# Kernel tuning notes

Hardware: AMD Instinct MI355X
Metric: run time of the kernel (lower is better)

Reference implementation:

```python
import jax, jax.numpy as jnp
import numpy as np

M, K, N = 4096, 4096, 4096

def setup_inputs() -> dict:
    key = jax.random.key(0)
    k1, k2, k3 = jax.random.split(key, 3)
    a = jax.random.randint(k1, (M, K), 0, 127, dtype=jnp.int32)
    b = jax.random.randint(k2, (K, N), 0, 127, dtype=jnp.int32)
    scale = jax.random.uniform(k3, (N,), dtype=jnp.float32)
    return {"a": a, "b": b, "scale": scale}

def reference(a, b, scale):
    a8 = a.astype(jnp.int8)
    b8 = b.astype(jnp.int8)
    acc = jnp.matmul(a8, b8, preferred_element_type=jnp.int32)  # [M, N] int32
    # fused per-column (per-output-channel) dequantization scale
    return acc.astype(jnp.float32) * scale[None, :]  # [M, N] float32
```

## Files before the change

### kernel.cpp

```cpp
#include <hip/hip_runtime.h>
#include <stdint.h>

#define M_DIM 4096
#define K_DIM 4096
#define N_DIM 4096

typedef int v4i __attribute__((ext_vector_type(4)));
typedef int int32x4 __attribute__((ext_vector_type(4)));

__device__ __forceinline__ void gload_lds16(const void* g, void* l) {
    __builtin_amdgcn_global_load_lds(
        (const __attribute__((address_space(1))) uint32_t*)g,
        (__attribute__((address_space(3))) uint32_t*)l, 16, 0, 0);
}

__global__ void pack_a_kernel(const int* __restrict__ a, char* __restrict__ a8, int total4) {
    int idx = blockIdx.x * blockDim.x + threadIdx.x;
    int stride = gridDim.x * blockDim.x;
    for (int i = idx; i < total4; i += stride) {
        int32x4 v = ((const int32x4*)a)[i];
        uint32_t p = (uint32_t)(v.x & 0xff) | ((uint32_t)(v.y & 0xff) << 8) |
                     ((uint32_t)(v.z & 0xff) << 16) | ((uint32_t)(v.w & 0xff) << 24);
        ((uint32_t*)a8)[i] = p;
    }
}

__global__ void pack_bt_kernel(const int* __restrict__ b, char* __restrict__ b8t) {
    __shared__ char tile[64][68];
    int k0 = blockIdx.y * 64;
    int n0 = blockIdx.x * 64;
    int tx = threadIdx.x & 63;
    int ty = threadIdx.x >> 6;
#pragma unroll
    for (int kk = 0; kk < 64; kk += 4) {
        tile[kk + ty][tx] = (char)b[(size_t)(k0 + kk + ty) * N_DIM + n0 + tx];
    }
    __syncthreads();
    int td = threadIdx.x & 15;
    int tn = threadIdx.x >> 4;
#pragma unroll
    for (int nn0 = 0; nn0 < 64; nn0 += 16) {
        int nn = nn0 + tn;
        uint32_t p = (uint32_t)(uint8_t)tile[td * 4 + 0][nn] |
                     ((uint32_t)(uint8_t)tile[td * 4 + 1][nn] << 8) |
                     ((uint32_t)(uint8_t)tile[td * 4 + 2][nn] << 16) |
                     ((uint32_t)(uint8_t)tile[td * 4 + 3][nn] << 24);
        *(uint32_t*)&b8t[(size_t)(n0 + nn) * K_DIM + k0 + td * 4] = p;
    }
}

#define BM 256
#define BN 256
#define BK 128
#define KTILES (K_DIM / BK)

#define BAR __builtin_amdgcn_s_barrier()
#define WAIT_LGKM asm volatile("s_waitcnt lgkmcnt(0)" ::: "memory")
#define WAIT_VM4 asm volatile("s_waitcnt vmcnt(4)" ::: "memory")
#define WAIT_VM0 asm volatile("s_waitcnt vmcnt(0)" ::: "memory")

#define DS_A(dst, kk, ib)                                                               \
    _Pragma("unroll") for (int i_ = 0; i_ < 4; ++i_) dst[i_] =                          \
        *(const v4i*)(lds + bufOff + (kk) * 16384 + aOff + ((ib) + i_) * 1024);

#define DS_B(dst, kk)                                                                   \
    _Pragma("unroll") for (int j_ = 0; j_ < 4; ++j_) dst[j_] =                          \
        *(const v4i*)(lds + bufOff + (kk) * 16384 + bOff + j_ * 1024);

#define MM(ib, AF, BF)                                                                  \
    __builtin_amdgcn_s_setprio(1);                                                      \
    _Pragma("unroll") for (int i_ = 0; i_ < 4; ++i_)                                    \
    _Pragma("unroll") for (int j_ = 0; j_ < 4; ++j_)                                    \
        acc[(ib) + i_][j_] =                                                            \
            __builtin_amdgcn_mfma_i32_16x16x64_i8(AF[i_], BF[j_], acc[(ib) + i_][j_],   \
                                                  0, 0, 0);                             \
    __builtin_amdgcn_s_setprio(0);

__global__ __launch_bounds__(512, 2) void gemm_i8_8ph(const char* __restrict__ A8,
                                                      const char* __restrict__ B8T,
                                                      const float* __restrict__ scale,
                                                      float* __restrict__ out) {
    __shared__ char lds[131072];

    int tid = threadIdx.x;
    int wave = tid >> 6;
    int lane = tid & 63;
    int wr = wave >> 2;
    int wc = wave & 3;
    int l15 = lane & 15;

    int bid = blockIdx.x;
    int swz = (bid & 7) * 32 + (bid >> 3);
    int bm = swz >> 4;
    int bn = swz & 15;

    int rA = tid >> 2;
    int cc = ((tid & 3) ^ ((tid >> 3) & 3)) << 4;
    const char* aSrc = A8 + (size_t)(bm * BM + rA) * K_DIM + cc;
    const char* bSrc = B8T + (size_t)(bn * BN + rA) * K_DIM + cc;

    int slot = (((lane >> 4) ^ ((lane >> 1) & 3)) << 4);
    int aOff = wr * 8192 + l15 * 64 + slot;
    int bOff = 32768 + wc * 4096 + l15 * 64 + slot;

    v4i acc[8][4];
#pragma unroll
    for (int i = 0; i < 8; ++i)
#pragma unroll
        for (int j = 0; j < 4; ++j) acc[i][j] = (v4i){0, 0, 0, 0};

    auto stage = [&](const char* srcBase, int kt1, int kk, int dstOff) {
        const char* s = srcBase + (size_t)kt1 * BK + kk * 64;
        char* d = (char*)lds + dstOff + wave * 1024;
        gload_lds16(s, d);
        gload_lds16(s + (size_t)128 * K_DIM, d + 8192);
    };

    stage(aSrc, 0, 0, 0);
    stage(bSrc, 0, 0, 32768);
    stage(aSrc, 0, 1, 16384);
    stage(bSrc, 0, 1, 49152);
    WAIT_VM4;
    BAR;

    int bufOff = 0;
    v4i aF[4], aG[4], bF[4];

    for (int kt = 0; kt < KTILES - 1; ++kt) {
        int nbufOff = bufOff ^ 65536;
        DS_A(aF, 0, 0);
        DS_B(bF, 0);
        stage(aSrc, kt + 1, 0, nbufOff + 0);
        BAR;
        WAIT_LGKM;
        MM(0, aF, bF);
        BAR;
        DS_A(aG, 0, 4);
        stage(bSrc, kt + 1, 0, nbufOff + 32768);
        BAR;
        WAIT_LGKM;
        MM(4, aG, bF);
        WAIT_VM4;
        BAR;
        DS_A(aF, 1, 0);
        DS_B(bF, 1);
        stage(aSrc, kt + 1, 1, nbufOff + 16384);
        BAR;
        WAIT_LGKM;
        MM(0, aF, bF);
        BAR;
        DS_A(aG, 1, 4);
        stage(bSrc, kt + 1, 1, nbufOff + 49152);
        BAR;
        WAIT_LGKM;
        MM(4, aG, bF);
        WAIT_VM4;
        BAR;
        bufOff = nbufOff;
    }

    DS_A(aF, 0, 0);
    DS_B(bF, 0);
    BAR;
    WAIT_LGKM;
    MM(0, aF, bF);
    BAR;
    DS_A(aG, 0, 4);
    BAR;
    WAIT_LGKM;
    MM(4, aG, bF);
    WAIT_VM0;
    BAR;
    DS_A(aF, 1, 0);
    DS_B(bF, 1);
    BAR;
    WAIT_LGKM;
    MM(0, aF, bF);
    BAR;
    DS_A(aG, 1, 4);
    WAIT_LGKM;
    MM(4, aG, bF);

    size_t orow0 = (size_t)bm * BM + wr * 128 + (lane >> 4) * 4;
    int ocol0 = bn * BN + wc * 64 + l15;
#pragma unroll
    for (int j = 0; j < 4; ++j) {
        int col = ocol0 + j * 16;
        float s = scale[col];
#pragma unroll
        for (int i = 0; i < 8; ++i) {
            size_t row = orow0 + (size_t)i * 16;
#pragma unroll
            for (int r = 0; r < 4; ++r) {
                out[(row + r) * N_DIM + col] = (float)acc[i][j][r] * s;
            }
        }
    }
}

#define FBM 128
#define FBN 128
#define FBK 64

__global__ __launch_bounds__(256) void gemm_i8_fused_kernel(const int* __restrict__ a,
                                                            const int* __restrict__ b,
                                                            const float* __restrict__ scale,
                                                            float* __restrict__ out) {
    __shared__ char As[FBM * FBK];
    __shared__ char Bs[FBN * FBK];

    int tid = threadIdx.x;
    int wave = tid >> 6;
    int lane = tid & 63;

    int nwg = gridDim.x;
    int cpx = nwg >> 3;
    int bid = blockIdx.x;
    int swz = (bid & 7) * cpx + (bid >> 3);
    int bm = swz >> 5;
    int bn = swz & 31;

    int f0 = tid * 16;
    int m0 = f0 >> 6;
    int k0 = f0 & 63;

    int nn = tid & 127;
    int kh = tid >> 7;

    int wr = wave >> 1;
    int wc = wave & 1;
    int lrow = lane & 15;
    int kgrp = (lane >> 4) * 16;

    v4i acc[4][4];
#pragma unroll
    for (int i = 0; i < 4; ++i)
#pragma unroll
        for (int j = 0; j < 4; ++j) acc[i][j] = (v4i){0, 0, 0, 0};

    const int kTiles = K_DIM / FBK;
    for (int kt = 0; kt < kTiles; ++kt) {
        __syncthreads();
#pragma unroll
        for (int r = 0; r < 2; ++r) {
            const int* src = a + (size_t)(bm * FBM + m0 + r * 64) * K_DIM + kt * FBK + k0;
            uint32_t pk[4];
#pragma unroll
            for (int q = 0; q < 4; ++q) {
                int32x4 v = *(const int32x4*)(src + q * 4);
                pk[q] = (uint32_t)(v.x & 0xff) | ((uint32_t)(v.y & 0xff) << 8) |
                        ((uint32_t)(v.z & 0xff) << 16) | ((uint32_t)(v.w & 0xff) << 24);
            }
            *(v4i*)&As[f0 + r * 4096] = (v4i){(int)pk[0], (int)pk[1], (int)pk[2], (int)pk[3]};
        }
#pragma unroll
        for (int d = 0; d < 8; ++d) {
            uint32_t p = 0;
#pragma unroll
            for (int i = 0; i < 4; ++i) {
                int kk = kt * FBK + kh * 32 + d * 4 + i;
                p |= (uint32_t)(b[(size_t)kk * N_DIM + bn * FBN + nn] & 0xff) << (8 * i);
            }
            *(uint32_t*)&Bs[nn * 64 + kh * 32 + d * 4] = p;
        }
        __syncthreads();

        v4i aF[4], bF[4];
#pragma unroll
        for (int i = 0; i < 4; ++i)
            aF[i] = *(const v4i*)&As[(wr * 64 + i * 16 + lrow) * FBK + kgrp];
#pragma unroll
        for (int j = 0; j < 4; ++j)
            bF[j] = *(const v4i*)&Bs[(wc * 64 + j * 16 + lrow) * FBK + kgrp];
#pragma unroll
        for (int i = 0; i < 4; ++i)
#pragma unroll
            for (int j = 0; j < 4; ++j)
                acc[i][j] = __builtin_amdgcn_mfma_i32_16x16x64_i8(aF[i], bF[j], acc[i][j], 0, 0, 0);
    }

    size_t orow0 = (size_t)bm * FBM + wr * 64;
    int ocol0 = bn * FBN + wc * 64;
#pragma unroll
    for (int j = 0; j < 4; ++j) {
        int col = ocol0 + j * 16 + lrow;
        float s = scale[col];
#pragma unroll
        for (int i = 0; i < 4; ++i) {
            size_t row = orow0 + i * 16 + (lane >> 4) * 4;
#pragma unroll
            for (int r = 0; r < 4; ++r) {
                out[(row + r) * N_DIM + col] = (float)acc[i][j][r] * s;
            }
        }
    }
}

extern "C" void kernel_launch(void* const* d_in, const int* in_sizes, int n_in,
                              void* d_out, int out_size, void* d_ws, size_t ws_size,
                              hipStream_t stream) {
    const int* a = (const int*)d_in[0];
    const int* b = (const int*)d_in[1];
    const float* scale = (const float*)d_in[2];
    float* out = (float*)d_out;

    size_t need = (size_t)M_DIM * K_DIM + (size_t)K_DIM * N_DIM;
    if (ws_size >= need) {
        char* a8 = (char*)d_ws;
        char* b8t = a8 + (size_t)M_DIM * K_DIM;
        pack_a_kernel<<<2048, 256, 0, stream>>>(a, a8, M_DIM * K_DIM / 4);
        pack_bt_kernel<<<dim3(64, 64), 256, 0, stream>>>(b, b8t);
        gemm_i8_8ph<<<256, 512, 0, stream>>>(a8, b8t, scale, out);
    } else {
        gemm_i8_fused_kernel<<<1024, 256, 0, stream>>>(a, b, scale, out);
    }
}
```

Measured before the change: 98.70 us.

## Merge pack kernels into one launch and prefetch LDS fragments across GEMM phases

Folds the A-pack and B-transpose-pack kernels into one launch with block-index dispatch, removing a launch and the serialization gap between them. The GEMM main loop now loads the next k-slice's A/B fragments from LDS into separate register sets before the current MFMA block runs. The explicit lgkmcnt waits are dropped and the load/MFMA ordering is left to the compiler, with fewer barriers around the MFMAs. This raises register pressure and relies on compiler-inserted waits for correctness of LDS reads against the async global->LDS stages.

```diff
diff --git a/kernel.cpp b/kernel.cpp
--- a/kernel.cpp
+++ b/kernel.cpp
@@ -14,38 +14,41 @@
         (__attribute__((address_space(3))) uint32_t*)l, 16, 0, 0);
 }
 
-__global__ void pack_a_kernel(const int* __restrict__ a, char* __restrict__ a8, int total4) {
-    int idx = blockIdx.x * blockDim.x + threadIdx.x;
-    int stride = gridDim.x * blockDim.x;
-    for (int i = idx; i < total4; i += stride) {
-        int32x4 v = ((const int32x4*)a)[i];
-        uint32_t p = (uint32_t)(v.x & 0xff) | ((uint32_t)(v.y & 0xff) << 8) |
-                     ((uint32_t)(v.z & 0xff) << 16) | ((uint32_t)(v.w & 0xff) << 24);
-        ((uint32_t*)a8)[i] = p;
-    }
-}
-
-__global__ void pack_bt_kernel(const int* __restrict__ b, char* __restrict__ b8t) {
+__global__ void pack_ab_kernel(const int* __restrict__ a, char* __restrict__ a8,
+                               const int* __restrict__ b, char* __restrict__ b8t) {
     __shared__ char tile[64][68];
-    int k0 = blockIdx.y * 64;
-    int n0 = blockIdx.x * 64;
-    int tx = threadIdx.x & 63;
-    int ty = threadIdx.x >> 6;
-#pragma unroll
-    for (int kk = 0; kk < 64; kk += 4) {
-        tile[kk + ty][tx] = (char)b[(size_t)(k0 + kk + ty) * N_DIM + n0 + tx];
-    }
-    __syncthreads();
-    int td = threadIdx.x & 15;
-    int tn = threadIdx.x >> 4;
-#pragma unroll
-    for (int nn0 = 0; nn0 < 64; nn0 += 16) {
-        int nn = nn0 + tn;
-        uint32_t p = (uint32_t)(uint8_t)tile[td * 4 + 0][nn] |
-                     ((uint32_t)(uint8_t)tile[td * 4 + 1][nn] << 8) |
-                     ((uint32_t)(uint8_t)tile[td * 4 + 2][nn] << 16) |
-                     ((uint32_t)(uint8_t)tile[td * 4 + 3][nn] << 24);
-        *(uint32_t*)&b8t[(size_t)(n0 + nn) * K_DIM + k0 + td * 4] = p;
+    if (blockIdx.x < 2048) {
+        int idx = blockIdx.x * 256 + threadIdx.x;
+        const int stride = 2048 * 256;
+        const int total4 = M_DIM * K_DIM / 4;
+        for (int i = idx; i < total4; i += stride) {
+            int32x4 v = ((const int32x4*)a)[i];
+            uint32_t p = (uint32_t)(v.x & 0xff) | ((uint32_t)(v.y & 0xff) << 8) |
+                         ((uint32_t)(v.z & 0xff) << 16) | ((uint32_t)(v.w & 0xff) << 24);
+            ((uint32_t*)a8)[i] = p;
+        }
+    } else {
+        int bid2 = blockIdx.x - 2048;
+        int n0 = (bid2 & 63) * 64;
+        int k0 = (bid2 >> 6) * 64;
+        int tx = threadIdx.x & 63;
+        int ty = threadIdx.x >> 6;
+#pragma unroll
+        for (int kk = 0; kk < 64; kk += 4) {
+            tile[kk + ty][tx] = (char)b[(size_t)(k0 + kk + ty) * N_DIM + n0 + tx];
+        }
+        __syncthreads();
+        int td = threadIdx.x & 15;
+        int tn = threadIdx.x >> 4;
+#pragma unroll
+        for (int nn0 = 0; nn0 < 64; nn0 += 16) {
+            int nn = nn0 + tn;
+            uint32_t p = (uint32_t)(uint8_t)tile[td * 4 + 0][nn] |
+                         ((uint32_t)(uint8_t)tile[td * 4 + 1][nn] << 8) |
+                         ((uint32_t)(uint8_t)tile[td * 4 + 2][nn] << 16) |
+                         ((uint32_t)(uint8_t)tile[td * 4 + 3][nn] << 24);
+            *(uint32_t*)&b8t[(size_t)(n0 + nn) * K_DIM + k0 + td * 4] = p;
+        }
     }
 }
 
@@ -55,8 +58,8 @@
 #define KTILES (K_DIM / BK)
 
 #define BAR __builtin_amdgcn_s_barrier()
-#define WAIT_LGKM asm volatile("s_waitcnt lgkmcnt(0)" ::: "memory")
 #define WAIT_VM4 asm volatile("s_waitcnt vmcnt(4)" ::: "memory")
+#define WAIT_VM2 asm volatile("s_waitcnt vmcnt(2)" ::: "memory")
 #define WAIT_VM0 asm volatile("s_waitcnt vmcnt(0)" ::: "memory")
 
 #define DS_A(dst, kk, ib)                                                               \
@@ -124,62 +127,50 @@
     BAR;
 
     int bufOff = 0;
-    v4i aF[4], aG[4], bF[4];
+    v4i a03[4], a47[4], b0[4];
+    v4i a03n[4], a47n[4], b0n[4];
 
     for (int kt = 0; kt < KTILES - 1; ++kt) {
         int nbufOff = bufOff ^ 65536;
-        DS_A(aF, 0, 0);
-        DS_B(bF, 0);
+        DS_A(a03, 0, 0);
+        DS_B(b0, 0);
+        DS_A(a47, 0, 4);
         stage(aSrc, kt + 1, 0, nbufOff + 0);
         BAR;
-        WAIT_LGKM;
-        MM(0, aF, bF);
-        BAR;
-        DS_A(aG, 0, 4);
+        MM(0, a03, b0);
+        WAIT_VM2;
+        BAR;
+        DS_A(a03n, 1, 0);
+        DS_B(b0n, 1);
         stage(bSrc, kt + 1, 0, nbufOff + 32768);
         BAR;
-        WAIT_LGKM;
-        MM(4, aG, bF);
+        MM(4, a47, b0);
+        BAR;
+        DS_A(a47n, 1, 4);
+        stage(aSrc, kt + 1, 1, nbufOff + 16384);
+        BAR;
+        MM(0, a03n, b0n);
+        BAR;
+        stage(bSrc, kt + 1, 1, nbufOff + 49152);
+        BAR;
+        MM(4, a47n, b0n);
         WAIT_VM4;
         BAR;
-        DS_A(aF, 1, 0);
-        DS_B(bF, 1);
-        stage(aSrc, kt + 1, 1, nbufOff + 16384);
-        BAR;
-        WAIT_LGKM;
-        MM(0, aF, bF);
-        BAR;
-        DS_A(aG, 1, 4);
-        stage(bSrc, kt + 1, 1, nbufOff + 49152);
-        BAR;
-        WAIT_LGKM;
-        MM(4, aG, bF);
-        WAIT_VM4;
-        BAR;
         bufOff = nbufOff;
     }
 
-    DS_A(aF, 0, 0);
-    DS_B(bF, 0);
-    BAR;
-    WAIT_LGKM;
-    MM(0, aF, bF);
-    BAR;
-    DS_A(aG, 0, 4);
-    BAR;
-    WAIT_LGKM;
-    MM(4, aG, bF);
+    DS_A(a03, 0, 0);
+    DS_B(b0, 0);
+    DS_A(a47, 0, 4);
+    MM(0, a03, b0);
+    MM(4, a47, b0);
     WAIT_VM0;
     BAR;
-    DS_A(aF, 1, 0);
-    DS_B(bF, 1);
-    BAR;
-    WAIT_LGKM;
-    MM(0, aF, bF);
-    BAR;
-    DS_A(aG, 1, 4);
-    WAIT_LGKM;
-    MM(4, aG, bF);
+    DS_A(a03n, 1, 0);
+    DS_B(b0n, 1);
+    DS_A(a47n, 1, 4);
+    MM(0, a03n, b0n);
+    MM(4, a47n, b0n);
 
     size_t orow0 = (size_t)bm * BM + wr * 128 + (lane >> 4) * 4;
     int ocol0 = bn * BN + wc * 64 + l15;
@@ -308,8 +299,7 @@
     if (ws_size >= need) {
         char* a8 = (char*)d_ws;
         char* b8t = a8 + (size_t)M_DIM * K_DIM;
-        pack_a_kernel<<<2048, 256, 0, stream>>>(a, a8, M_DIM * K_DIM / 4);
-        pack_bt_kernel<<<dim3(64, 64), 256, 0, stream>>>(b, b8t);
+        pack_ab_kernel<<<2048 + 4096, 256, 0, stream>>>(a, a8, b, b8t);
         gemm_i8_8ph<<<256, 512, 0, stream>>>(a8, b8t, scale, out);
     } else {
         gemm_i8_fused_kernel<<<1024, 256, 0, stream>>>(a, b, scale, out);
```

Result: faster. 95.94 us (-2.8%).
